# Optimization experiments

Measured on AMD Instinct MI355X. Metric: run time of the kernel, lower is better.

Reference implementation:

```python
import jax, jax.numpy as jnp
import numpy as np

B, H, W, C = 8, 256, 256, 256


def setup_inputs() -> dict:
    key = jax.random.key(0)
    ks = jax.random.split(key, 5)
    scale = 1.0 / np.sqrt(C)
    return {
        "x": jax.random.normal(ks[0], (B, H, W, C), dtype=jnp.float32),
        "wq": jax.random.normal(ks[1], (C, C), dtype=jnp.float32) * scale,
        "bq": jnp.zeros((C,), dtype=jnp.float32),
        "wk": jax.random.normal(ks[2], (C, C), dtype=jnp.float32) * scale,
        "bk": jnp.zeros((C,), dtype=jnp.float32),
        "wv": jax.random.normal(ks[3], (C, C), dtype=jnp.float32) * scale,
        "bv": jnp.zeros((C,), dtype=jnp.float32),
        "gamma": jax.random.normal(ks[4], (C,), dtype=jnp.float32) * scale,
    }


def reference(x, wq, bq, wk, bk, wv, bv, gamma):
    # 1x1 convs == per-pixel channel matmuls
    q = jnp.einsum("bhwc,cd->bhwd", x, wq) + bq  # [B,H,W,C]
    k = jnp.einsum("bhwc,cd->bhwd", x, wk) + bk
    v = jnp.einsum("bhwc,cd->bhwd", x, wv) + bv
    # tf.matmul(q, k, transpose_b=True) on 4D: batch dims (B,H), attention over W
    attn = jax.nn.softmax(jnp.einsum("bhic,bhjc->bhij", q, k), axis=-1)  # [B,H,W,W]
    out = jnp.einsum("bhij,bhjc->bhic", attn, v)  # [B,H,W,C]
    return gamma * out + x
```

## Files before the change

### kernel.cpp

```cpp
#include <hip/hip_runtime.h>
#include <hip/hip_bf16.h>


#define NPAIR 2048
#define SEQ 256
#define DIM 256
#define XSTR 264
#define SCRSTR 48

typedef __attribute__((ext_vector_type(8))) short bf16x8;
typedef __attribute__((ext_vector_type(4))) float f32x4;

__device__ __forceinline__ unsigned short f2bf(float f) {
  union { float f; unsigned u; } v; v.f = f;
  unsigned r = v.u + 0x7FFFu + ((v.u >> 16) & 1u);
  return (unsigned short)(r >> 16);
}

__global__ void prep_kernel(const float* __restrict__ wq, const float* __restrict__ bq,
                            const float* __restrict__ wk, const float* __restrict__ wv,
                            unsigned short* __restrict__ MT, unsigned short* __restrict__ WvT,
                            float* __restrict__ u) {
  int b = blockIdx.x, t = threadIdx.x;
  if (b < 256) {
    int r = b;
    for (int c = t; c < 256; c += blockDim.x) {
      float acc = 0.f;
      for (int d = 0; d < 256; ++d) acc += wq[c * 256 + d] * wk[r * 256 + d];
      MT[r * 256 + c] = f2bf(acc);
    }
  } else if (b == 256) {
    for (int cc = t; cc < 256; cc += blockDim.x) {
      float acc = 0.f;
      for (int d = 0; d < 256; ++d) acc += wk[cc * 256 + d] * bq[d];
      u[cc] = acc;
    }
  } else {
    int r = b - 257;
    for (int c = t; c < 256; c += blockDim.x) WvT[r * 256 + c] = f2bf(wv[c * 256 + r]);
  }
}

__global__ __launch_bounds__(512, 2)
void attn_scores_kernel(const float* __restrict__ x, const unsigned short* __restrict__ MT,
                        const float* __restrict__ u, float* __restrict__ out) {
  __shared__ unsigned short Xs[SEQ * XSTR];
  __shared__ unsigned short Yscr[8][16 * SCRSTR];
  const int p = blockIdx.x;
  const long xbase = (long)p * (SEQ * DIM);
  const int tid = threadIdx.x;
  const int wid = tid >> 6;
  const int ln = tid & 63;
  const int l16 = ln & 15;
  const int quad = ln >> 4;

  for (int it = 0; it < 64; ++it) {
    int idx = 2 * (tid + 512 * it);
    float2 v = *(const float2*)(x + xbase + idx);
    int j = idx >> 8, c = idx & 255;
    unsigned pack = (unsigned)f2bf(v.x) | ((unsigned)f2bf(v.y) << 16);
    *(unsigned*)&Xs[j * XSTR + c] = pack;
  }
  __syncthreads();

  float ureg[16];
#pragma unroll
  for (int nt = 0; nt < 16; ++nt) ureg[nt] = u[nt * 16 + l16];

  unsigned short* Aout =
      (unsigned short*)((char*)out + (size_t)p * (SEQ * DIM * 4) + 131072);
  unsigned short* scr = &Yscr[wid][0];

  for (int ch = 0; ch < 2; ++ch) {
    const int chunk = wid + 8 * ch;
    const int i0 = chunk * 16;

    f32x4 acc[16];
#pragma unroll
    for (int nt = 0; nt < 16; ++nt) acc[nt] = (f32x4){0.f, 0.f, 0.f, 0.f};
#pragma unroll
    for (int ks = 0; ks < 8; ++ks) {
      bf16x8 a = *(const bf16x8*)&Xs[(i0 + l16) * XSTR + ks * 32 + quad * 8];
#pragma unroll
      for (int nt = 0; nt < 16; ++nt) {
        bf16x8 b = *(const bf16x8*)&MT[(nt * 16 + l16) * 256 + ks * 32 + quad * 8];
        acc[nt] = __builtin_amdgcn_mfma_f32_16x16x32_bf16(a, b, acc[nt], 0, 0, 0);
      }
    }

    f32x4 sacc[16];
#pragma unroll
    for (int mt = 0; mt < 16; ++mt) sacc[mt] = (f32x4){0.f, 0.f, 0.f, 0.f};
#pragma unroll
    for (int e = 0; e < 8; ++e) {
      asm volatile("s_waitcnt lgkmcnt(0)" ::: "memory");
#pragma unroll
      for (int h = 0; h < 2; ++h) {
        int nt = 2 * e + h;
#pragma unroll
        for (int r = 0; r < 4; ++r) {
          float yv = acc[nt][r] + ureg[nt];
          scr[(quad * 4 + r) * SCRSTR + h * 16 + l16] = f2bf(yv);
        }
      }
      asm volatile("s_waitcnt lgkmcnt(0)" ::: "memory");
      bf16x8 bfrag = *(const bf16x8*)&scr[l16 * SCRSTR + quad * 8];
#pragma unroll
      for (int mt = 0; mt < 16; ++mt) {
        bf16x8 a = *(const bf16x8*)&Xs[(mt * 16 + l16) * XSTR + e * 32 + quad * 8];
        sacc[mt] = __builtin_amdgcn_mfma_f32_16x16x32_bf16(a, bfrag, sacc[mt], 0, 0, 0);
      }
    }

    float mx = -1e30f;
#pragma unroll
    for (int mt = 0; mt < 16; ++mt)
#pragma unroll
      for (int r = 0; r < 4; ++r) mx = fmaxf(mx, sacc[mt][r]);
    mx = fmaxf(mx, __shfl_xor(mx, 16, 64));
    mx = fmaxf(mx, __shfl_xor(mx, 32, 64));
    float sum = 0.f;
#pragma unroll
    for (int mt = 0; mt < 16; ++mt)
#pragma unroll
      for (int r = 0; r < 4; ++r) {
        float ev = exp2f((sacc[mt][r] - mx) * 1.44269504088896340736f);
        sacc[mt][r] = ev;
        sum += ev;
      }
    sum += __shfl_xor(sum, 16, 64);
    sum += __shfl_xor(sum, 32, 64);
    float rs = 1.0f / sum;

#pragma unroll
    for (int mt = 0; mt < 16; ++mt)
#pragma unroll
      for (int r = 0; r < 4; ++r) {
        int j = mt * 16 + quad * 4 + r;
        Aout[(i0 + l16) * 256 + j] = f2bf(sacc[mt][r] * rs);
      }
  }
}

__global__ __launch_bounds__(512, 2)
void attn_out_kernel(const float* __restrict__ x, const unsigned short* __restrict__ WvT,
                     const float* __restrict__ bv, const float* __restrict__ gamma,
                     float* __restrict__ out) {
  __shared__ unsigned short Vs[DIM * XSTR];
  const int p = blockIdx.x;
  const long xbase = (long)p * (SEQ * DIM);
  const int tid = threadIdx.x;
  const int wid = tid >> 6;
  const int ln = tid & 63;
  const int l16 = ln & 15;
  const int quad = ln >> 4;
  unsigned short* Aslot =
      (unsigned short*)((char*)out + (size_t)p * (SEQ * DIM * 4) + 131072);

  bf16x8 afr[8];
  {
    int i = 16 * wid + l16;
#pragma unroll
    for (int ks = 0; ks < 8; ++ks)
      afr[ks] = *(const bf16x8*)&Aslot[i * 256 + ks * 32 + quad * 8];
  }

  {
    f32x4 vacc[16][2];
#pragma unroll
    for (int mt = 0; mt < 16; ++mt) {
      vacc[mt][0] = (f32x4){0.f, 0.f, 0.f, 0.f};
      vacc[mt][1] = (f32x4){0.f, 0.f, 0.f, 0.f};
    }
#pragma unroll
    for (int ks = 0; ks < 8; ++ks) {
      bf16x8 bfr[2];
#pragma unroll
      for (int nt = 0; nt < 2; ++nt) {
        const float* xp = x + xbase + (long)(32 * wid + nt * 16 + l16) * 256 + ks * 32 + quad * 8;
        float4 x0 = *(const float4*)xp;
        float4 x1 = *(const float4*)(xp + 4);
        union { bf16x8 v; unsigned short s[8]; } uu;
        uu.s[0] = f2bf(x0.x); uu.s[1] = f2bf(x0.y); uu.s[2] = f2bf(x0.z); uu.s[3] = f2bf(x0.w);
        uu.s[4] = f2bf(x1.x); uu.s[5] = f2bf(x1.y); uu.s[6] = f2bf(x1.z); uu.s[7] = f2bf(x1.w);
        bfr[nt] = uu.v;
      }
#pragma unroll
      for (int mt = 0; mt < 16; ++mt) {
        bf16x8 a = *(const bf16x8*)&WvT[(mt * 16 + l16) * 256 + ks * 32 + quad * 8];
        vacc[mt][0] = __builtin_amdgcn_mfma_f32_16x16x32_bf16(a, bfr[0], vacc[mt][0], 0, 0, 0);
        vacc[mt][1] = __builtin_amdgcn_mfma_f32_16x16x32_bf16(a, bfr[1], vacc[mt][1], 0, 0, 0);
      }
    }
#pragma unroll
    for (int mt = 0; mt < 16; ++mt)
#pragma unroll
      for (int r = 0; r < 4; ++r) {
        int d = mt * 16 + quad * 4 + r;
        float bvv = bv[d];
#pragma unroll
        for (int nt = 0; nt < 2; ++nt) {
          int j = 32 * wid + nt * 16 + l16;
          Vs[d * XSTR + j] = f2bf(vacc[mt][nt][r] + bvv);
        }
      }
  }
  float greg[16];
#pragma unroll
  for (int nt = 0; nt < 16; ++nt) greg[nt] = gamma[nt * 16 + l16];
  __syncthreads();

  float* outp = out + (size_t)p * (SEQ * DIM);
  for (int rnd = 0; rnd < 2; ++rnd) {
    const int i0 = (wid + 8 * rnd) * 16;
    f32x4 oacc[16];
#pragma unroll
    for (int nt = 0; nt < 16; ++nt) oacc[nt] = (f32x4){0.f, 0.f, 0.f, 0.f};
#pragma unroll
    for (int ks = 0; ks < 8; ++ks) {
      bf16x8 a = afr[ks];
#pragma unroll
      for (int nt = 0; nt < 16; ++nt) {
        bf16x8 b = *(const bf16x8*)&Vs[(nt * 16 + l16) * XSTR + ks * 32 + quad * 8];
        oacc[nt] = __builtin_amdgcn_mfma_f32_16x16x32_bf16(a, b, oacc[nt], 0, 0, 0);
      }
    }
    if (rnd == 0) {
      int i = 16 * (8 + wid) + l16;
#pragma unroll
      for (int ks = 0; ks < 8; ++ks)
        afr[ks] = *(const bf16x8*)&Aslot[i * 256 + ks * 32 + quad * 8];
      asm volatile("s_waitcnt vmcnt(0)" ::: "memory");
      __syncthreads();
    }
#pragma unroll
    for (int nt = 0; nt < 16; ++nt)
#pragma unroll
      for (int r = 0; r < 4; ++r) {
        int i = i0 + quad * 4 + r;
        int dd = nt * 16 + l16;
        float xv = x[xbase + (long)i * 256 + dd];
        outp[(long)i * 256 + dd] = greg[nt] * oacc[nt][r] + xv;
      }
  }
}

extern "C" void kernel_launch(void* const* d_in, const int* in_sizes, int n_in,
                              void* d_out, int out_size, void* d_ws, size_t ws_size,
                              hipStream_t stream) {
  const float* x     = (const float*)d_in[0];
  const float* wq    = (const float*)d_in[1];
  const float* bq    = (const float*)d_in[2];
  const float* wk    = (const float*)d_in[3];
  const float* wv    = (const float*)d_in[5];
  const float* bv    = (const float*)d_in[6];
  const float* gamma = (const float*)d_in[7];
  float* out = (float*)d_out;

  unsigned short* MT  = (unsigned short*)d_ws;
  unsigned short* WvT = MT + 65536;
  float* u            = (float*)(WvT + 65536);

  prep_kernel<<<513, 256, 0, stream>>>(wq, bq, wk, wv, MT, WvT, u);
  attn_scores_kernel<<<NPAIR, 512, 0, stream>>>(x, MT, u, out);
  attn_out_kernel<<<NPAIR, 512, 0, stream>>>(x, WvT, bv, gamma, out);
}
```

Baseline: 2.649 ms.

## Fuse score and output kernels, computing V from shared-memory bf16 x

Merges the attention-score kernel and the output kernel into one launch per (b,h) pair. V is now computed from the bf16 copy of x already held in LDS rather than by re-reading fp32 x from global memory, and the result overwrites that same LDS buffer. The bias on V moves algebraically into the epilogue, which is valid because softmax rows sum to one. The probability matrix is written through a per-wave LDS transpose to get coalesced 16-byte stores. The costs are a second kernel launch and a duplicate global read of x, traded for higher register pressure (the 64-entry pay array) and extra barriers in a single, longer kernel.

```diff
diff --git a/kernel.cpp b/kernel.cpp
--- a/kernel.cpp
+++ b/kernel.cpp
@@ -1,5 +1,4 @@
 #include <hip/hip_runtime.h>
-#include <hip/hip_bf16.h>
 
 
 #define NPAIR 2048
@@ -10,11 +9,16 @@
 
 typedef __attribute__((ext_vector_type(8))) short bf16x8;
 typedef __attribute__((ext_vector_type(4))) float f32x4;
+typedef __attribute__((ext_vector_type(4))) unsigned uint4v;
+typedef __attribute__((ext_vector_type(2))) unsigned uint2v;
 
 __device__ __forceinline__ unsigned short f2bf(float f) {
   union { float f; unsigned u; } v; v.f = f;
   unsigned r = v.u + 0x7FFFu + ((v.u >> 16) & 1u);
   return (unsigned short)(r >> 16);
+}
+__device__ __forceinline__ unsigned pack2(float a, float b) {
+  return (unsigned)f2bf(a) | ((unsigned)f2bf(b) << 16);
 }
 
 __global__ void prep_kernel(const float* __restrict__ wq, const float* __restrict__ bq,
@@ -42,8 +46,10 @@
 }
 
 __global__ __launch_bounds__(512, 2)
-void attn_scores_kernel(const float* __restrict__ x, const unsigned short* __restrict__ MT,
-                        const float* __restrict__ u, float* __restrict__ out) {
+void attn_fused_kernel(const float* __restrict__ x, const unsigned short* __restrict__ MT,
+                       const float* __restrict__ u, const unsigned short* __restrict__ WvT,
+                       const float* __restrict__ bv, const float* __restrict__ gamma,
+                       float* __restrict__ out) {
   __shared__ unsigned short Xs[SEQ * XSTR];
   __shared__ unsigned short Yscr[8][16 * SCRSTR];
   const int p = blockIdx.x;
@@ -133,81 +139,66 @@
     float rs = 1.0f / sum;
 
 #pragma unroll
-    for (int mt = 0; mt < 16; ++mt)
-#pragma unroll
-      for (int r = 0; r < 4; ++r) {
-        int j = mt * 16 + quad * 4 + r;
-        Aout[(i0 + l16) * 256 + j] = f2bf(sacc[mt][r] * rs);
-      }
-  }
-}
-
-__global__ __launch_bounds__(512, 2)
-void attn_out_kernel(const float* __restrict__ x, const unsigned short* __restrict__ WvT,
-                     const float* __restrict__ bv, const float* __restrict__ gamma,
-                     float* __restrict__ out) {
-  __shared__ unsigned short Vs[DIM * XSTR];
-  const int p = blockIdx.x;
-  const long xbase = (long)p * (SEQ * DIM);
-  const int tid = threadIdx.x;
-  const int wid = tid >> 6;
-  const int ln = tid & 63;
-  const int l16 = ln & 15;
-  const int quad = ln >> 4;
-  unsigned short* Aslot =
-      (unsigned short*)((char*)out + (size_t)p * (SEQ * DIM * 4) + 131072);
+    for (int ks = 0; ks < 8; ++ks) {
+      asm volatile("s_waitcnt lgkmcnt(0)" ::: "memory");
+#pragma unroll
+      for (int h = 0; h < 2; ++h) {
+        int mt = 2 * ks + h;
+        unsigned lo = pack2(sacc[mt][0] * rs, sacc[mt][1] * rs);
+        unsigned hi = pack2(sacc[mt][2] * rs, sacc[mt][3] * rs);
+        *(unsigned*)&scr[l16 * SCRSTR + h * 16 + quad * 4] = lo;
+        *(unsigned*)&scr[l16 * SCRSTR + h * 16 + quad * 4 + 2] = hi;
+      }
+      asm volatile("s_waitcnt lgkmcnt(0)" ::: "memory");
+      uint4v t = *(const uint4v*)&scr[(ln >> 2) * SCRSTR + (ln & 3) * 8];
+      *(uint4v*)&Aout[(i0 + (ln >> 2)) * 256 + ks * 32 + (ln & 3) * 8] = t;
+    }
+  }
+  __syncthreads();
 
   bf16x8 afr[8];
   {
     int i = 16 * wid + l16;
 #pragma unroll
     for (int ks = 0; ks < 8; ++ks)
-      afr[ks] = *(const bf16x8*)&Aslot[i * 256 + ks * 32 + quad * 8];
-  }
-
-  {
-    f32x4 vacc[16][2];
-#pragma unroll
-    for (int mt = 0; mt < 16; ++mt) {
-      vacc[mt][0] = (f32x4){0.f, 0.f, 0.f, 0.f};
-      vacc[mt][1] = (f32x4){0.f, 0.f, 0.f, 0.f};
-    }
-#pragma unroll
-    for (int ks = 0; ks < 8; ++ks) {
-      bf16x8 bfr[2];
-#pragma unroll
-      for (int nt = 0; nt < 2; ++nt) {
-        const float* xp = x + xbase + (long)(32 * wid + nt * 16 + l16) * 256 + ks * 32 + quad * 8;
-        float4 x0 = *(const float4*)xp;
-        float4 x1 = *(const float4*)(xp + 4);
-        union { bf16x8 v; unsigned short s[8]; } uu;
-        uu.s[0] = f2bf(x0.x); uu.s[1] = f2bf(x0.y); uu.s[2] = f2bf(x0.z); uu.s[3] = f2bf(x0.w);
-        uu.s[4] = f2bf(x1.x); uu.s[5] = f2bf(x1.y); uu.s[6] = f2bf(x1.z); uu.s[7] = f2bf(x1.w);
-        bfr[nt] = uu.v;
-      }
-#pragma unroll
-      for (int mt = 0; mt < 16; ++mt) {
-        bf16x8 a = *(const bf16x8*)&WvT[(mt * 16 + l16) * 256 + ks * 32 + quad * 8];
-        vacc[mt][0] = __builtin_amdgcn_mfma_f32_16x16x32_bf16(a, bfr[0], vacc[mt][0], 0, 0, 0);
-        vacc[mt][1] = __builtin_amdgcn_mfma_f32_16x16x32_bf16(a, bfr[1], vacc[mt][1], 0, 0, 0);
-      }
-    }
-#pragma unroll
-    for (int mt = 0; mt < 16; ++mt)
-#pragma unroll
-      for (int r = 0; r < 4; ++r) {
-        int d = mt * 16 + quad * 4 + r;
-        float bvv = bv[d];
-#pragma unroll
-        for (int nt = 0; nt < 2; ++nt) {
-          int j = 32 * wid + nt * 16 + l16;
-          Vs[d * XSTR + j] = f2bf(vacc[mt][nt][r] + bvv);
-        }
-      }
-  }
-  float greg[16];
-#pragma unroll
-  for (int nt = 0; nt < 16; ++nt) greg[nt] = gamma[nt * 16 + l16];
+      afr[ks] = *(const bf16x8*)&Aout[i * 256 + ks * 32 + quad * 8];
+  }
+
+  unsigned pay[64];
+#pragma unroll
+  for (int dc = 0; dc < 16; ++dc) {
+    bf16x8 bfr[8];
+#pragma unroll
+    for (int ks = 0; ks < 8; ++ks)
+      bfr[ks] = *(const bf16x8*)&WvT[(dc * 16 + l16) * 256 + ks * 32 + quad * 8];
+#pragma unroll
+    for (int jr = 0; jr < 2; ++jr) {
+      const int jc = wid + 8 * jr;
+      f32x4 vacc = (f32x4){0.f, 0.f, 0.f, 0.f};
+#pragma unroll
+      for (int ks = 0; ks < 8; ++ks) {
+        bf16x8 a = *(const bf16x8*)&Xs[(jc * 16 + l16) * XSTR + ks * 32 + quad * 8];
+        vacc = __builtin_amdgcn_mfma_f32_16x16x32_bf16(a, bfr[ks], vacc, 0, 0, 0);
+      }
+      pay[dc * 4 + jr * 2 + 0] = pack2(vacc[0], vacc[1]);
+      pay[dc * 4 + jr * 2 + 1] = pack2(vacc[2], vacc[3]);
+    }
+  }
+  __syncthreads();
+#pragma unroll
+  for (int dc = 0; dc < 16; ++dc)
+#pragma unroll
+    for (int jr = 0; jr < 2; ++jr) {
+      const int jc = wid + 8 * jr;
+      uint2v w = {pay[dc * 4 + jr * 2], pay[dc * 4 + jr * 2 + 1]};
+      *(uint2v*)&Xs[(dc * 16 + l16) * XSTR + jc * 16 + quad * 4] = w;
+    }
+  float greg[16], bvreg[16];
+#pragma unroll
+  for (int nt = 0; nt < 16; ++nt) {
+    greg[nt] = gamma[nt * 16 + l16];
+    bvreg[nt] = bv[nt * 16 + l16];
+  }
   __syncthreads();
 
   float* outp = out + (size_t)p * (SEQ * DIM);
@@ -221,7 +212,7 @@
       bf16x8 a = afr[ks];
 #pragma unroll
       for (int nt = 0; nt < 16; ++nt) {
-        bf16x8 b = *(const bf16x8*)&Vs[(nt * 16 + l16) * XSTR + ks * 32 + quad * 8];
+        bf16x8 b = *(const bf16x8*)&Xs[(nt * 16 + l16) * XSTR + ks * 32 + quad * 8];
         oacc[nt] = __builtin_amdgcn_mfma_f32_16x16x32_bf16(a, b, oacc[nt], 0, 0, 0);
       }
     }
@@ -229,7 +220,7 @@
       int i = 16 * (8 + wid) + l16;
 #pragma unroll
       for (int ks = 0; ks < 8; ++ks)
-        afr[ks] = *(const bf16x8*)&Aslot[i * 256 + ks * 32 + quad * 8];
+        afr[ks] = *(const bf16x8*)&Aout[i * 256 + ks * 32 + quad * 8];
       asm volatile("s_waitcnt vmcnt(0)" ::: "memory");
       __syncthreads();
     }
@@ -240,7 +231,7 @@
         int i = i0 + quad * 4 + r;
         int dd = nt * 16 + l16;
         float xv = x[xbase + (long)i * 256 + dd];
-        outp[(long)i * 256 + dd] = greg[nt] * oacc[nt][r] + xv;
+        outp[(long)i * 256 + dd] = greg[nt] * (oacc[nt][r] + bvreg[nt]) + xv;
       }
   }
 }
@@ -262,6 +253,5 @@
   float* u            = (float*)(WvT + 65536);
 
   prep_kernel<<<513, 256, 0, stream>>>(wq, bq, wk, wv, MT, WvT, u);
-  attn_scores_kernel<<<NPAIR, 512, 0, stream>>>(x, MT, u, out);
-  attn_out_kernel<<<NPAIR, 512, 0, stream>>>(x, WvT, bv, gamma, out);
-}
+  attn_fused_kernel<<<NPAIR, 512, 0, stream>>>(x, MT, u, WvT, bv, gamma, out);
+}
```

New measurement: 2.457 ms. 1.08x faster.
